# Kernel tuning notes

Measured on AMD Instinct MI355X. Metric: run time of the kernel, lower is better.

The kernel has to match this reference:

```python
import jax, jax.numpy as jnp
import numpy as np


def _qkernel(r, i, j, k):
    # Build the real-valued block kernel of a quaternion dense layer.
    # r,i,j,k: [in/4, out/4] -> kernel [in, out] implementing the Hamilton product.
    col_r = jnp.concatenate([r, -i, -j, -k], axis=0)
    col_i = jnp.concatenate([i, r, -k, j], axis=0)
    col_j = jnp.concatenate([j, k, r, -i], axis=0)
    col_k = jnp.concatenate([k, -j, i, r], axis=0)
    return jnp.concatenate([col_r, col_i, col_j, col_k], axis=1)


def setup_inputs() -> dict:
    key = jax.random.key(0)
    ks = jax.random.split(key, 12)
    B, F, H = 32768, 1024, 256
    F4, H4 = F // 4, H // 4
    s_in = 1.0 / np.sqrt(F)
    s_h = 1.0 / np.sqrt(H)
    inp = {
        "x": jax.random.normal(ks[0], (B, F), dtype=jnp.float32),
        "wx_r": jax.random.normal(ks[1], (4, F4, H4), dtype=jnp.float32) * s_in,
        "wx_i": jax.random.normal(ks[2], (4, F4, H4), dtype=jnp.float32) * s_in,
        "wx_j": jax.random.normal(ks[3], (4, F4, H4), dtype=jnp.float32) * s_in,
        "wx_k": jax.random.normal(ks[4], (4, F4, H4), dtype=jnp.float32) * s_in,
        "bx": jnp.zeros((4, H), dtype=jnp.float32),
        "uh_r": jax.random.normal(ks[5], (4, H4, H4), dtype=jnp.float32) * s_h,
        "uh_i": jax.random.normal(ks[6], (4, H4, H4), dtype=jnp.float32) * s_h,
        "uh_j": jax.random.normal(ks[7], (4, H4, H4), dtype=jnp.float32) * s_h,
        "uh_k": jax.random.normal(ks[8], (4, H4, H4), dtype=jnp.float32) * s_h,
        "fco_w": jax.random.normal(ks[9], (H, H), dtype=jnp.float32) * s_h,
        "fco_b": jnp.zeros((H,), dtype=jnp.float32),
    }
    return inp


def reference(x, wx_r, wx_i, wx_j, wx_k, bx, uh_r, uh_i, uh_j, uh_k, fco_w, fco_b):
    # Single-step quaternion LSTM cell with zero initial hidden/cell state.
    # Gate order along leading axis: [forget, input, output, cell].
    Kx = jax.vmap(_qkernel)(wx_r, wx_i, wx_j, wx_k)   # [4, F, H]
    Ku = jax.vmap(_qkernel)(uh_r, uh_i, uh_j, uh_k)   # [4, H, H]
    H = bx.shape[1]
    h0 = jnp.zeros((x.shape[0], H), dtype=x.dtype)
    c0 = h0
    gx = jnp.einsum('bf,gfh->gbh', x, Kx) + bx[:, None, :]   # [4, B, H]
    gu = jnp.einsum('bh,ghk->gbk', h0, Ku)                    # [4, B, H]
    z = gx + gu
    ft = jax.nn.sigmoid(z[0])
    it = jax.nn.sigmoid(z[1])
    ot = jax.nn.sigmoid(z[2])
    at = z[3]
    c = it * jnp.tanh(at) + ft * c0
    h = ot * jnp.tanh(c)
    return h @ fco_w + fco_b
```

## Files before the change

### kernel.cpp

```cpp
#include <hip/hip_runtime.h>
#include <cstdint>
#include <cstddef>

#define WS_WP   0
#define WS_FCO  1572864
#define WS_BP   1703936
#define WS_HVP  1707008

typedef __attribute__((ext_vector_type(8))) __bf16 bf16x8;
typedef __attribute__((ext_vector_type(4))) float floatx4;

__device__ __forceinline__ unsigned short f2bf(float f) {
  unsigned int u = __builtin_bit_cast(unsigned int, f);
  u += 0x7fffu + ((u >> 16) & 1u);
  return (unsigned short)(u >> 16);
}

__device__ __forceinline__ float sigmf(float z) {
  return __builtin_amdgcn_rcpf(1.f + __expf(-z));
}
__device__ __forceinline__ float tanh_(float z) {
  return 1.f - 2.f * __builtin_amdgcn_rcpf(1.f + __expf(2.f * z));
}

__device__ __forceinline__ void gld16(const void* g, void* l) {
  __builtin_amdgcn_global_load_lds(
      (const __attribute__((address_space(1))) unsigned int*)g,
      (__attribute__((address_space(3))) unsigned int*)l, 16, 0, 0);
}

__global__ __launch_bounds__(256) void pack_k(
    const float* __restrict__ wr, const float* __restrict__ wi,
    const float* __restrict__ wj, const float* __restrict__ wk,
    const float* __restrict__ bx, const float* __restrict__ fw,
    unsigned short* __restrict__ Wp, unsigned short* __restrict__ Fp,
    float* __restrict__ bp) {
  int t = threadIdx.x;
  if (blockIdx.x < 384) {
    int gpp = blockIdx.x >> 7;
    int oct = blockIdx.x & 127;
    int gp = gpp + 1;
    int h = t;
    int hb = h >> 6, hr = h & 63;
    int f0 = oct << 3;
    int fb = f0 >> 8, fr0 = f0 & 255;
    const int   comp_t[4][4] = {{0,1,2,3},{1,0,3,2},{2,3,0,1},{3,2,1,0}};
    const float sign_t[4][4] = {{1.f,-1.f,-1.f,-1.f},{1.f,1.f,-1.f,1.f},
                                {1.f,1.f,1.f,-1.f},{1.f,-1.f,1.f,1.f}};
    const float* srcs[4] = {wr, wi, wj, wk};
    const float* s = srcs[comp_t[hb][fb]] + ((size_t)((gp << 8) + fr0)) * 64 + hr;
    float sg = sign_t[hb][fb];
    unsigned short v[8];
#pragma unroll
    for (int j = 0; j < 8; ++j) v[j] = f2bf(sg * s[(size_t)j * 64]);
    int c = h * 3 + gpp;
    int cb = c / 96, nl = c % 96;
    int kb = oct >> 2, q = oct & 3;
    int idx16 = (nl << 2) + (q ^ ((nl >> 1) & 3));
    uint4 val = make_uint4(
        (unsigned)v[0] | ((unsigned)v[1] << 16), (unsigned)v[2] | ((unsigned)v[3] << 16),
        (unsigned)v[4] | ((unsigned)v[5] << 16), (unsigned)v[6] | ((unsigned)v[7] << 16));
    *(uint4*)(Wp + (size_t)(cb * 32 + kb) * 3072 + idx16 * 8) = val;
    if (oct == 0) bp[c] = bx[(gp << 8) + h];
  } else {
    int oct = blockIdx.x - 384;
    int n = t;
    int k0 = oct << 3;
    unsigned short v[8];
#pragma unroll
    for (int j = 0; j < 8; ++j) v[j] = f2bf(fw[(size_t)(k0 + j) * 256 + n]);
    int nb = n >> 7, nl = n & 127, kb = oct >> 2, q = oct & 3;
    int idx16 = (nl << 2) + (q ^ ((nl >> 1) & 3));
    uint4 val = make_uint4(
        (unsigned)v[0] | ((unsigned)v[1] << 16), (unsigned)v[2] | ((unsigned)v[3] << 16),
        (unsigned)v[4] | ((unsigned)v[5] << 16), (unsigned)v[6] | ((unsigned)v[7] << 16));
    *(uint4*)(Fp + (size_t)((nb << 3) + kb) * 4096 + idx16 * 8) = val;
  }
}

__global__ __launch_bounds__(256, 4) void gemm1_k(
    const float* __restrict__ x, const unsigned short* __restrict__ Wp,
    const float* __restrict__ bp, unsigned short* __restrict__ hvp) {
  __shared__ char smem[22528];
  float* sAf = (float*)smem;
  unsigned short* sBs = (unsigned short*)(smem + 16384);
  float* zep = (float*)smem;

  const int t = threadIdx.x;
  const int lane = t & 63, wid = t >> 6;
  const int wm = wid >> 1, wn = wid & 1;
  const int lrow = lane & 15, q = lane >> 4;
  const int row0 = blockIdx.x * 128;
  const int cby = blockIdx.y;
  const float* xbase = x + (size_t)row0 * 1024;

  floatx4 acc[4][3];
#pragma unroll
  for (int i = 0; i < 4; ++i)
#pragma unroll
    for (int j = 0; j < 3; ++j) acc[i][j] = (floatx4){0.f, 0.f, 0.f, 0.f};

  for (int kt = 0; kt < 32; ++kt) {
    const int k0 = kt * 32;
#pragma unroll
    for (int i = 0; i < 4; ++i) {
      int s = t + i * 256;
      int m = s >> 3, j = s & 7, jj = j ^ (m & 7);
      gld16(xbase + (size_t)m * 1024 + k0 + jj * 4, sAf + s * 4);
    }
    const unsigned short* bt = Wp + (size_t)(cby * 32 + kt) * 3072;
    gld16(bt + t * 8, sBs + t * 8);
    if (t < 128) gld16(bt + 2048 + t * 8, sBs + 2048 + t * 8);
    __syncthreads();
    bf16x8 af[4], bf[3];
#pragma unroll
    for (int mt = 0; mt < 4; ++mt) {
      int m = wm * 64 + mt * 16 + lrow;
      const float4 a0 = *(const float4*)(sAf + (m * 8 + ((2 * q) ^ (m & 7))) * 4);
      const float4 a1 = *(const float4*)(sAf + (m * 8 + ((2 * q + 1) ^ (m & 7))) * 4);
      bf16x8 v;
      v[0] = (__bf16)a0.x; v[1] = (__bf16)a0.y; v[2] = (__bf16)a0.z; v[3] = (__bf16)a0.w;
      v[4] = (__bf16)a1.x; v[5] = (__bf16)a1.y; v[6] = (__bf16)a1.z; v[7] = (__bf16)a1.w;
      af[mt] = v;
    }
#pragma unroll
    for (int nt = 0; nt < 3; ++nt) {
      int n = wn * 48 + nt * 16 + lrow;
      int off16 = (n << 2) + (q ^ ((n >> 1) & 3));
      bf[nt] = *(const bf16x8*)(const void*)(sBs + off16 * 8);
    }
#pragma unroll
    for (int mt = 0; mt < 4; ++mt)
#pragma unroll
      for (int nt = 0; nt < 3; ++nt)
        acc[mt][nt] = __builtin_amdgcn_mfma_f32_16x16x32_bf16(af[mt], bf[nt], acc[mt][nt], 0, 0, 0);
    __syncthreads();
  }

  const float* bp0 = bp + cby * 96;
  const int row_ip = t >> 3, ho = t & 7;
  unsigned short* hvt = hvp + (size_t)(blockIdx.x * 8 + cby) * 4096;
#pragma unroll
  for (int p = 0; p < 4; ++p) {
    if (wm == (p >> 1)) {
#pragma unroll
      for (int mt2 = 0; mt2 < 2; ++mt2) {
        int mt = (p & 1) * 2 + mt2;
#pragma unroll
        for (int nt = 0; nt < 3; ++nt)
#pragma unroll
          for (int r = 0; r < 4; ++r)
            zep[(mt2 * 16 + q * 4 + r) * 100 + wn * 48 + nt * 16 + lrow] = acc[mt][nt][r];
      }
    }
    __syncthreads();
    unsigned short v[4];
#pragma unroll
    for (int j = 0; j < 4; ++j) {
      int hl = ho * 4 + j;
      float zi = zep[row_ip * 100 + hl * 3 + 0] + bp0[hl * 3 + 0];
      float zo = zep[row_ip * 100 + hl * 3 + 1] + bp0[hl * 3 + 1];
      float zc = zep[row_ip * 100 + hl * 3 + 2] + bp0[hl * 3 + 2];
      float it = sigmf(zi);
      float ot = sigmf(zo);
      float cc = it * tanh_(zc);
      v[j] = f2bf(ot * tanh_(cc));
    }
    int ml = p * 32 + row_ip;
    int qq = ho >> 1;
    int idx16 = (ml << 2) + (qq ^ ((ml >> 1) & 3));
    uint2 val = make_uint2((unsigned)v[0] | ((unsigned)v[1] << 16),
                           (unsigned)v[2] | ((unsigned)v[3] << 16));
    *(uint2*)(hvt + (size_t)idx16 * 8 + (ho & 1) * 4) = val;
    __syncthreads();
  }
}

__global__ __launch_bounds__(256, 4) void gemm2_k(
    const unsigned short* __restrict__ hvp, const unsigned short* __restrict__ Fp,
    const float* __restrict__ fcob, float* __restrict__ out) {
  __shared__ unsigned short sB[32768];
  const int t = threadIdx.x;
  const int lane = t & 63, wid = t >> 6;
  const int wm = wid >> 1, wn = wid & 1;
  const int lrow = lane & 15, q = lane >> 4;
  const int mb = blockIdx.x, nb = blockIdx.y;

  const unsigned short* fpb = Fp + (size_t)nb * 32768;
#pragma unroll
  for (int i = 0; i < 16; ++i) gld16(fpb + (t + i * 256) * 8, sB + (t + i * 256) * 8);

  floatx4 acc[4][4];
#pragma unroll
  for (int i = 0; i < 4; ++i)
#pragma unroll
    for (int j = 0; j < 4; ++j) acc[i][j] = (floatx4){0.f, 0.f, 0.f, 0.f};
  __syncthreads();

#pragma unroll
  for (int kt = 0; kt < 8; ++kt) {
    const unsigned short* at_ = hvp + (size_t)(mb * 8 + kt) * 4096;
    bf16x8 af[4], bf[4];
#pragma unroll
    for (int mt = 0; mt < 4; ++mt) {
      int m = wm * 64 + mt * 16 + lrow;
      int o = (m << 2) + (q ^ ((m >> 1) & 3));
      af[mt] = *(const bf16x8*)(const void*)(at_ + o * 8);
    }
#pragma unroll
    for (int nt = 0; nt < 4; ++nt) {
      int n = wn * 64 + nt * 16 + lrow;
      int o = (n << 2) + (q ^ ((n >> 1) & 3));
      bf[nt] = *(const bf16x8*)(const void*)(sB + kt * 4096 + o * 8);
    }
#pragma unroll
    for (int mt = 0; mt < 4; ++mt)
#pragma unroll
      for (int nt = 0; nt < 4; ++nt)
        acc[mt][nt] = __builtin_amdgcn_mfma_f32_16x16x32_bf16(af[mt], bf[nt], acc[mt][nt], 0, 0, 0);
  }
#pragma unroll
  for (int nt = 0; nt < 4; ++nt) {
    int colg = nb * 128 + wn * 64 + nt * 16 + lrow;
    float bias = fcob[colg];
#pragma unroll
    for (int mt = 0; mt < 4; ++mt) {
      int rowg = mb * 128 + wm * 64 + mt * 16 + q * 4;
#pragma unroll
      for (int r = 0; r < 4; ++r)
        out[(size_t)(rowg + r) * 256 + colg] = acc[mt][nt][r] + bias;
    }
  }
}

extern "C" void kernel_launch(void* const* d_in, const int* in_sizes, int n_in,
                              void* d_out, int out_size, void* d_ws, size_t ws_size,
                              hipStream_t stream) {
  const float* x  = (const float*)d_in[0];
  const float* wr = (const float*)d_in[1];
  const float* wi = (const float*)d_in[2];
  const float* wj = (const float*)d_in[3];
  const float* wk = (const float*)d_in[4];
  const float* bx = (const float*)d_in[5];
  const float* fw = (const float*)d_in[10];
  const float* fb = (const float*)d_in[11];
  char* ws = (char*)d_ws;
  unsigned short* Wp  = (unsigned short*)(ws + WS_WP);
  unsigned short* Fp  = (unsigned short*)(ws + WS_FCO);
  float*          bp  = (float*)(ws + WS_BP);
  unsigned short* hvp = (unsigned short*)(ws + WS_HVP);
  float*          out = (float*)d_out;

  hipLaunchKernelGGL(pack_k,  dim3(416),    dim3(256), 0, stream, wr, wi, wj, wk, bx, fw, Wp, Fp, bp);
  hipLaunchKernelGGL(gemm1_k, dim3(256, 8), dim3(256), 0, stream, x, Wp, bp, hvp);
  hipLaunchKernelGGL(gemm2_k, dim3(256, 2), dim3(256), 0, stream, hvp, Fp, fb, out);
}
```

Measured before the change: 308.7 us.

## Widen gemm1 N-tile, load operands directly to registers with double buffering

The gate GEMM now computes 192 gate columns per block instead of 96, so x is re-read from memory half as often. The weight packing is rearranged to match. Shared-memory staging is removed: each wave loads its x fragments and packed weights straight from global memory into registers, double-buffered across k steps, with no per-iteration barriers. The grid is reordered so the column blocks sharing a row tile run next to each other for L2 reuse. The cost is higher register use (occupancy bound lowered to 2) and uncoalesced direct global loads of fp32 x rows.

```diff
diff --git a/kernel.cpp b/kernel.cpp
--- a/kernel.cpp
+++ b/kernel.cpp
@@ -54,13 +54,13 @@
 #pragma unroll
     for (int j = 0; j < 8; ++j) v[j] = f2bf(sg * s[(size_t)j * 64]);
     int c = h * 3 + gpp;
-    int cb = c / 96, nl = c % 96;
+    int cb = c / 192, nl = c % 192;
     int kb = oct >> 2, q = oct & 3;
     int idx16 = (nl << 2) + (q ^ ((nl >> 1) & 3));
     uint4 val = make_uint4(
         (unsigned)v[0] | ((unsigned)v[1] << 16), (unsigned)v[2] | ((unsigned)v[3] << 16),
         (unsigned)v[4] | ((unsigned)v[5] << 16), (unsigned)v[6] | ((unsigned)v[7] << 16));
-    *(uint4*)(Wp + (size_t)(cb * 32 + kb) * 3072 + idx16 * 8) = val;
+    *(uint4*)(Wp + (size_t)(cb * 32 + kb) * 6144 + idx16 * 8) = val;
     if (oct == 0) bp[c] = bx[(gp << 8) + h];
   } else {
     int oct = blockIdx.x - 384;
@@ -78,100 +78,112 @@
   }
 }
 
-__global__ __launch_bounds__(256, 4) void gemm1_k(
+__global__ __launch_bounds__(256, 2) void gemm1_k(
     const float* __restrict__ x, const unsigned short* __restrict__ Wp,
     const float* __restrict__ bp, unsigned short* __restrict__ hvp) {
-  __shared__ char smem[22528];
-  float* sAf = (float*)smem;
-  unsigned short* sBs = (unsigned short*)(smem + 16384);
-  float* zep = (float*)smem;
+  __shared__ float zep[64 * 201];
 
   const int t = threadIdx.x;
   const int lane = t & 63, wid = t >> 6;
   const int wm = wid >> 1, wn = wid & 1;
   const int lrow = lane & 15, q = lane >> 4;
-  const int row0 = blockIdx.x * 128;
-  const int cby = blockIdx.y;
-  const float* xbase = x + (size_t)row0 * 1024;
-
-  floatx4 acc[4][3];
+  const int cby = blockIdx.x;
+  const int rowt = blockIdx.y;
+  const int row0 = rowt * 128;
+
+  const float* xw = x + (size_t)(row0 + wm * 64 + lrow) * 1024 + q * 8;
+  const unsigned short* wpb = Wp + (size_t)cby * 32 * 6144;
+
+  int boff[6];
+#pragma unroll
+  for (int nt = 0; nt < 6; ++nt) {
+    int n = wn * 96 + nt * 16 + lrow;
+    boff[nt] = (n * 4 + (q ^ ((n >> 1) & 3))) * 8;
+  }
+
+  float4 a[2][4][2];
+  bf16x8 b[2][6];
+  floatx4 acc[4][6];
 #pragma unroll
   for (int i = 0; i < 4; ++i)
 #pragma unroll
-    for (int j = 0; j < 3; ++j) acc[i][j] = (floatx4){0.f, 0.f, 0.f, 0.f};
-
+    for (int j = 0; j < 6; ++j) acc[i][j] = (floatx4){0.f, 0.f, 0.f, 0.f};
+
+#pragma unroll
+  for (int mt = 0; mt < 4; ++mt) {
+    const float* p = xw + (size_t)mt * 16 * 1024;
+    a[0][mt][0] = *(const float4*)(p);
+    a[0][mt][1] = *(const float4*)(p + 4);
+  }
+#pragma unroll
+  for (int nt = 0; nt < 6; ++nt)
+    b[0][nt] = *(const bf16x8*)(const void*)(wpb + boff[nt]);
+
+#pragma unroll
   for (int kt = 0; kt < 32; ++kt) {
-    const int k0 = kt * 32;
-#pragma unroll
-    for (int i = 0; i < 4; ++i) {
-      int s = t + i * 256;
-      int m = s >> 3, j = s & 7, jj = j ^ (m & 7);
-      gld16(xbase + (size_t)m * 1024 + k0 + jj * 4, sAf + s * 4);
-    }
-    const unsigned short* bt = Wp + (size_t)(cby * 32 + kt) * 3072;
-    gld16(bt + t * 8, sBs + t * 8);
-    if (t < 128) gld16(bt + 2048 + t * 8, sBs + 2048 + t * 8);
+    const int cur = kt & 1, nxt = cur ^ 1;
+    if (kt < 31) {
+      const float* xk = xw + (kt + 1) * 32;
+      const unsigned short* bt = wpb + (size_t)(kt + 1) * 6144;
+#pragma unroll
+      for (int mt = 0; mt < 4; ++mt) {
+        const float* p = xk + (size_t)mt * 16 * 1024;
+        a[nxt][mt][0] = *(const float4*)(p);
+        a[nxt][mt][1] = *(const float4*)(p + 4);
+      }
+#pragma unroll
+      for (int nt = 0; nt < 6; ++nt)
+        b[nxt][nt] = *(const bf16x8*)(const void*)(bt + boff[nt]);
+    }
+#pragma unroll
+    for (int mt = 0; mt < 4; ++mt) {
+      const float4 a0 = a[cur][mt][0], a1 = a[cur][mt][1];
+      bf16x8 av;
+      av[0] = (__bf16)a0.x; av[1] = (__bf16)a0.y; av[2] = (__bf16)a0.z; av[3] = (__bf16)a0.w;
+      av[4] = (__bf16)a1.x; av[5] = (__bf16)a1.y; av[6] = (__bf16)a1.z; av[7] = (__bf16)a1.w;
+#pragma unroll
+      for (int nt = 0; nt < 6; ++nt)
+        acc[mt][nt] = __builtin_amdgcn_mfma_f32_16x16x32_bf16(av, b[cur][nt], acc[mt][nt], 0, 0, 0);
+    }
+  }
+
+  const float* bp0 = bp + cby * 192;
+  const int er = t >> 2, oc = t & 3;
+#pragma unroll
+  for (int pass = 0; pass < 2; ++pass) {
+    if (wm == pass) {
+#pragma unroll
+      for (int mt = 0; mt < 4; ++mt)
+#pragma unroll
+        for (int nt = 0; nt < 6; ++nt)
+#pragma unroll
+          for (int r = 0; r < 4; ++r)
+            zep[(mt * 16 + q * 4 + r) * 201 + wn * 96 + nt * 16 + lrow] = acc[mt][nt][r];
+    }
     __syncthreads();
-    bf16x8 af[4], bf[3];
-#pragma unroll
-    for (int mt = 0; mt < 4; ++mt) {
-      int m = wm * 64 + mt * 16 + lrow;
-      const float4 a0 = *(const float4*)(sAf + (m * 8 + ((2 * q) ^ (m & 7))) * 4);
-      const float4 a1 = *(const float4*)(sAf + (m * 8 + ((2 * q + 1) ^ (m & 7))) * 4);
-      bf16x8 v;
-      v[0] = (__bf16)a0.x; v[1] = (__bf16)a0.y; v[2] = (__bf16)a0.z; v[3] = (__bf16)a0.w;
-      v[4] = (__bf16)a1.x; v[5] = (__bf16)a1.y; v[6] = (__bf16)a1.z; v[7] = (__bf16)a1.w;
-      af[mt] = v;
-    }
-#pragma unroll
-    for (int nt = 0; nt < 3; ++nt) {
-      int n = wn * 48 + nt * 16 + lrow;
-      int off16 = (n << 2) + (q ^ ((n >> 1) & 3));
-      bf[nt] = *(const bf16x8*)(const void*)(sBs + off16 * 8);
-    }
-#pragma unroll
-    for (int mt = 0; mt < 4; ++mt)
-#pragma unroll
-      for (int nt = 0; nt < 3; ++nt)
-        acc[mt][nt] = __builtin_amdgcn_mfma_f32_16x16x32_bf16(af[mt], bf[nt], acc[mt][nt], 0, 0, 0);
-    __syncthreads();
-  }
-
-  const float* bp0 = bp + cby * 96;
-  const int row_ip = t >> 3, ho = t & 7;
-  unsigned short* hvt = hvp + (size_t)(blockIdx.x * 8 + cby) * 4096;
-#pragma unroll
-  for (int p = 0; p < 4; ++p) {
-    if (wm == (p >> 1)) {
-#pragma unroll
-      for (int mt2 = 0; mt2 < 2; ++mt2) {
-        int mt = (p & 1) * 2 + mt2;
-#pragma unroll
-        for (int nt = 0; nt < 3; ++nt)
-#pragma unroll
-          for (int r = 0; r < 4; ++r)
-            zep[(mt2 * 16 + q * 4 + r) * 100 + wn * 48 + nt * 16 + lrow] = acc[mt][nt][r];
+    int ml = pass * 64 + er;
+#pragma unroll
+    for (int half = 0; half < 2; ++half) {
+      int oo = oc + half * 4;
+      unsigned short v[8];
+#pragma unroll
+      for (int j = 0; j < 8; ++j) {
+        int hl = oo * 8 + j;
+        float zi = zep[er * 201 + hl * 3 + 0] + bp0[hl * 3 + 0];
+        float zo = zep[er * 201 + hl * 3 + 1] + bp0[hl * 3 + 1];
+        float zc = zep[er * 201 + hl * 3 + 2] + bp0[hl * 3 + 2];
+        float it = sigmf(zi);
+        float ot = sigmf(zo);
+        float cc = it * tanh_(zc);
+        v[j] = f2bf(ot * tanh_(cc));
       }
-    }
-    __syncthreads();
-    unsigned short v[4];
-#pragma unroll
-    for (int j = 0; j < 4; ++j) {
-      int hl = ho * 4 + j;
-      float zi = zep[row_ip * 100 + hl * 3 + 0] + bp0[hl * 3 + 0];
-      float zo = zep[row_ip * 100 + hl * 3 + 1] + bp0[hl * 3 + 1];
-      float zc = zep[row_ip * 100 + hl * 3 + 2] + bp0[hl * 3 + 2];
-      float it = sigmf(zi);
-      float ot = sigmf(zo);
-      float cc = it * tanh_(zc);
-      v[j] = f2bf(ot * tanh_(cc));
-    }
-    int ml = p * 32 + row_ip;
-    int qq = ho >> 1;
-    int idx16 = (ml << 2) + (qq ^ ((ml >> 1) & 3));
-    uint2 val = make_uint2((unsigned)v[0] | ((unsigned)v[1] << 16),
-                           (unsigned)v[2] | ((unsigned)v[3] << 16));
-    *(uint2*)(hvt + (size_t)idx16 * 8 + (ho & 1) * 4) = val;
+      int ktile = cby * 2 + (oo >> 2), qq = oo & 3;
+      int idx16 = (ml << 2) + (qq ^ ((ml >> 1) & 3));
+      uint4 val = make_uint4(
+          (unsigned)v[0] | ((unsigned)v[1] << 16), (unsigned)v[2] | ((unsigned)v[3] << 16),
+          (unsigned)v[4] | ((unsigned)v[5] << 16), (unsigned)v[6] | ((unsigned)v[7] << 16));
+      *(uint4*)(hvp + (size_t)(rowt * 8 + ktile) * 4096 + idx16 * 8) = val;
+    }
     __syncthreads();
   }
 }
@@ -252,6 +264,6 @@
   float*          out = (float*)d_out;
 
   hipLaunchKernelGGL(pack_k,  dim3(416),    dim3(256), 0, stream, wr, wi, wj, wk, bx, fw, Wp, Fp, bp);
-  hipLaunchKernelGGL(gemm1_k, dim3(256, 8), dim3(256), 0, stream, x, Wp, bp, hvp);
+  hipLaunchKernelGGL(gemm1_k, dim3(4, 256), dim3(256), 0, stream, x, Wp, bp, hvp);
   hipLaunchKernelGGL(gemm2_k, dim3(256, 2), dim3(256), 0, stream, hvp, Fp, fb, out);
 }
```

Result: slower. 381.4 us (+23.6%).
